# Kernel tuning notes

Measured on AMD Instinct MI355X. Metric: run time of the kernel, lower is better.

## Reference

```python
import jax, jax.numpy as jnp
import numpy as np

SEGMENT_LENGTHS = (2048, 4096, 8192)
DILATION_RATES = (1, 2, 4)


def setup_inputs() -> dict:
    key = jax.random.key(0)
    kq, kk, kv = jax.random.split(key, 3)
    b, n, h, d = 1, 8192, 12, 64
    q = jax.random.normal(kq, (b, n, h, d), dtype=jnp.float32)
    k = jax.random.normal(kk, (b, n, h, d), dtype=jnp.float32)
    v = jax.random.normal(kv, (b, n, h, d), dtype=jnp.float32)
    return {"q": q, "k": k, "v": v, "is_causal": 1}


def _dilated_attention(q, k, v, is_causal):
    # q, k, v: [b, n, h, d]
    b, n, h, d = q.shape
    num_groups = len(SEGMENT_LENGTHS)
    gh = h // num_groups  # heads per group
    scale = 1.0 / jnp.sqrt(jnp.asarray(d, dtype=q.dtype))
    qt = jnp.swapaxes(q, 1, 2)  # [b, h, n, d]
    kt = jnp.swapaxes(k, 1, 2)
    vt = jnp.swapaxes(v, 1, 2)
    group_outputs = []
    for i, (s, r) in enumerate(zip(SEGMENT_LENGTHS, DILATION_RATES)):
        hs, he = i * gh, (i + 1) * gh
        nseg = n // s
        # [b, gh, nseg, s, d]
        qs = qt[:, hs:he].reshape(b, gh, nseg, s, d)
        ks = kt[:, hs:he].reshape(b, gh, nseg, s, d)
        vs = vt[:, hs:he].reshape(b, gh, nseg, s, d)
        offset = i % r
        idx = offset + r * jnp.arange(s // r)  # dilated positions within segment
        qd = qs[:, :, :, idx]  # [b, gh, nseg, s//r, d]
        kd = ks[:, :, :, idx]
        vd = vs[:, :, :, idx]
        scores = jnp.einsum("bgnqd,bgnkd->bgnqk", qd, kd) * scale
        if is_causal:
            mask = idx[:, None] >= idx[None, :]  # same dilated indices for q/k
            scores = jnp.where(mask, scores, -jnp.inf)
        attn = jax.nn.softmax(scores, axis=-1)
        od = jnp.einsum("bgnqk,bgnkd->bgnqd", attn, vd)
        # scatter back into full segment; non-dilated positions output zero
        og = jnp.zeros((b, gh, nseg, s, d), dtype=q.dtype).at[:, :, :, idx].set(od)
        group_outputs.append(og.reshape(b, gh, n, d))
    out = jnp.concatenate(group_outputs, axis=1)  # [b, h, n, d]
    return jnp.swapaxes(out, 1, 2)  # [b, n, h, d]


def reference(q, k, v, is_causal):
    return _dilated_attention(q, k, v, bool(is_causal))
```

## Files before the change

kernel.cpp:

```cpp
#include <hip/hip_runtime.h>

typedef __attribute__((ext_vector_type(8))) __bf16 bf16x8;
typedef __attribute__((ext_vector_type(4))) __bf16 bf16x4;
typedef __attribute__((ext_vector_type(2))) __bf16 bf16x2;
typedef __attribute__((ext_vector_type(4))) float f32x4;

#define LOG2E 1.44269504088896f
#define KSWZ(t) (((t) & 7) << 4)
#define VSWZ(d) ((((d) & 7) ^ (((d) >> 3) & 7)) << 4)


__device__ __forceinline__ void inst_decode(int inst, int& head, int& sstart,
                                            int& r, int& off)
{
    if (inst < 16)      { head = inst & 3;          sstart = (inst >> 2) * 2048; r = 1; off = 0; }
    else if (inst < 24) { int j = inst - 16; head = 4 + (j & 3); sstart = (j >> 2) * 4096; r = 2; off = 1; }
    else                { head = 8 + (inst - 24);   sstart = 0;                  r = 4; off = 2; }
}

__global__ __launch_bounds__(512)
void dilattn_partial(const float* __restrict__ Qg, const float* __restrict__ Kg,
                     const float* __restrict__ Vg, float* __restrict__ Og,
                     char* __restrict__ ws, const int* __restrict__ causal_p)
{
    const int bid  = blockIdx.x;
    const int unit = (bid & 7) * 140 + (bid >> 3);
    const int inst = unit / 40;
    const int u    = 39 - (unit % 40);
    int qt, c;
    if (u < 4) { qt = u; c = 0; }
    else {
        int v = u - 4;
        if (v < 8)       { qt = 4 + (v >> 1); c = v & 1; }
        else if (v < 20) { int t = v - 8; int q3 = t / 3; qt = 8 + q3; c = t - 3 * q3; }
        else             { int t = v - 20; qt = 12 + (t >> 2); c = t & 3; }
    }
    int head, sstart, r, off;
    inst_decode(inst, head, sstart, r, off);

    const int causal = *causal_p;
    int kt_begin, kt_end;
    bool direct;
    if (causal) {
        int nkt = 2 * qt + 2;
        kt_begin = c * 8;
        kt_end   = (kt_begin + 8 < nkt) ? kt_begin + 8 : nkt;
        direct   = (qt < 4);
    } else {
        if (c) return;
        kt_begin = 0; kt_end = 32; direct = true;
    }

    const int tid  = threadIdx.x;
    const int lane = tid & 63;
    const int wave = tid >> 6;
    const int l15  = lane & 15;
    const int lhi  = lane >> 4;

    __shared__ char KV[16384];
    __shared__ __bf16 P_lds[8][16 * 64];

    const int qrow_base = qt * 128 + wave * 16;
    const float qscale = 0.125f * LOG2E;
    bf16x8 qfrag[2];
    {
        int qr = qrow_base + l15;
        long qtok = sstart + off + (long)r * qr;
        const float* qp = Qg + qtok * 768 + head * 64 + lhi * 8;
#pragma unroll
        for (int dc = 0; dc < 2; dc++) {
            f32x4 a = *(const f32x4*)(qp + dc * 32);
            f32x4 b = *(const f32x4*)(qp + dc * 32 + 4);
#pragma unroll
            for (int j = 0; j < 4; j++) {
                qfrag[dc][j]     = (__bf16)(a[j] * qscale);
                qfrag[dc][4 + j] = (__bf16)(b[j] * qscale);
            }
        }
    }

    f32x4 acc[4] = {};
    float m_run = -INFINITY;
    float l_run = 0.f;

    const bool isK = (wave < 4);
    const int t2   = tid & 255;
    const int tokK = t2 >> 2, q4 = t2 & 3;
    const int tokP = t2 >> 3, d8 = (t2 & 7) * 8;

    f32x4 r0, r1, r2, r3;

    const long gstep = (long)r * 64 * 768;
    const long vrow  = (long)r * 768;
    const float* gp0;
    {
        long tb = sstart + off + (long)r * (kt_begin * 64);
        gp0 = isK ? (Kg + (tb + (long)r * tokK) * 768 + head * 64 + q4 * 16)
                  : (Vg + (tb + (long)r * 2 * tokP) * 768 + head * 64 + d8);
    }

#define LOAD_STEP() do {                                                       \
        if (isK) {                                                             \
            r0 = *(const f32x4*)(gp0);      r1 = *(const f32x4*)(gp0 + 4);     \
            r2 = *(const f32x4*)(gp0 + 8);  r3 = *(const f32x4*)(gp0 + 12);    \
        } else {                                                               \
            const float* g1_ = gp0 + vrow;                                     \
            r0 = *(const f32x4*)(gp0);      r1 = *(const f32x4*)(gp0 + 4);     \
            r2 = *(const f32x4*)(g1_);      r3 = *(const f32x4*)(g1_ + 4);     \
        }                                                                      \
        gp0 += gstep;                                                          \
    } while (0)

#define STORE_TILE() do {                                                      \
        if (isK) {                                                             \
            char* Kb_ = KV;                                                    \
            bf16x8 w0_, w1_;                                                   \
            _Pragma("unroll")                                                  \
            for (int j = 0; j < 4; j++) {                                      \
                w0_[j] = (__bf16)r0[j]; w0_[4 + j] = (__bf16)r1[j];            \
                w1_[j] = (__bf16)r2[j]; w1_[4 + j] = (__bf16)r3[j];            \
            }                                                                  \
            int kb_ = tokK * 128 + q4 * 32;                                    \
            *(bf16x8*)(Kb_ + ((kb_)      ^ KSWZ(tokK))) = w0_;                 \
            *(bf16x8*)(Kb_ + ((kb_ + 16) ^ KSWZ(tokK))) = w1_;                 \
        } else {                                                               \
            char* Vb_ = KV + 8192;                                             \
            _Pragma("unroll")                                                  \
            for (int j = 0; j < 4; j++) {                                      \
                int d_ = d8 + j;                                               \
                bf16x2 wa_; wa_[0] = (__bf16)r0[j]; wa_[1] = (__bf16)r2[j];    \
                *(bf16x2*)(Vb_ + ((d_ * 128 + tokP * 4) ^ VSWZ(d_))) = wa_;    \
                int d2_ = d8 + 4 + j;                                          \
                bf16x2 wb_; wb_[0] = (__bf16)r1[j]; wb_[1] = (__bf16)r3[j];    \
                *(bf16x2*)(Vb_ + ((d2_ * 128 + tokP * 4) ^ VSWZ(d2_))) = wb_;  \
            }                                                                  \
        }                                                                      \
    } while (0)

    LOAD_STEP();
    STORE_TILE();
    __syncthreads();

    for (int kt = kt_begin; kt < kt_end; kt++) {
        const bool pf = (kt + 1 < kt_end);
        if (pf) LOAD_STEP();

        char* Kb = KV;
        char* Vb = KV + 8192;

        f32x4 s[4];
        __builtin_amdgcn_s_setprio(1);
#pragma unroll
        for (int nt = 0; nt < 4; nt++) {
            f32x4 cc = {};
#pragma unroll
            for (int dc = 0; dc < 2; dc++) {
                int krow = nt * 16 + l15;
                const bf16x8 kf = *(const bf16x8*)(Kb +
                    ((krow * 128 + dc * 64 + lhi * 16) ^ KSWZ(krow)));
                cc = __builtin_amdgcn_mfma_f32_16x16x32_bf16(kf, qfrag[dc], cc, 0, 0, 0);
            }
            s[nt] = cc;
        }
        __builtin_amdgcn_s_setprio(0);

        if (causal && (kt >> 1) == qt) {
            const int kofs = kt * 64 - qt * 128 - wave * 16;
#pragma unroll
            for (int nt = 0; nt < 4; nt++)
#pragma unroll
                for (int reg = 0; reg < 4; reg++)
                    if (kofs + nt * 16 + lhi * 4 + reg > l15)
                        s[nt][reg] = -INFINITY;
        }

        float a0 = fmaxf(fmaxf(s[0][0], s[0][1]), s[0][2]);
        float a1 = fmaxf(fmaxf(s[0][3], s[1][0]), s[1][1]);
        float a2 = fmaxf(fmaxf(s[1][2], s[1][3]), s[2][0]);
        float a3 = fmaxf(fmaxf(s[2][1], s[2][2]), s[2][3]);
        float a4 = fmaxf(fmaxf(s[3][0], s[3][1]), s[3][2]);
        float b0 = fmaxf(fmaxf(a0, a1), a2);
        float b1 = fmaxf(fmaxf(a3, a4), s[3][3]);
        float mt = fmaxf(b0, b1);
        mt = fmaxf(mt, __shfl_xor(mt, 16));
        mt = fmaxf(mt, __shfl_xor(mt, 32));
        if (!__all(mt - m_run <= 8.0f)) {
            float mn = fmaxf(m_run, mt);
            float sc = exp2f(m_run - mn);
            l_run *= sc;
            float scr[4];
#pragma unroll
            for (int reg = 0; reg < 4; reg++) scr[reg] = __shfl(sc, lhi * 4 + reg);
#pragma unroll
            for (int dt = 0; dt < 4; dt++)
#pragma unroll
                for (int reg = 0; reg < 4; reg++) acc[dt][reg] *= scr[reg];
            m_run = mn;
        }
        float psn[4];
#pragma unroll
        for (int nt = 0; nt < 4; nt++) {
            float p0 = exp2f(s[nt][0] - m_run);
            float p1 = exp2f(s[nt][1] - m_run);
            float p2 = exp2f(s[nt][2] - m_run);
            float p3 = exp2f(s[nt][3] - m_run);
            s[nt][0] = p0; s[nt][1] = p1; s[nt][2] = p2; s[nt][3] = p3;
            psn[nt] = (p0 + p1) + (p2 + p3);
        }
        float ps = (psn[0] + psn[1]) + (psn[2] + psn[3]);
        ps += __shfl_xor(ps, 16);
        ps += __shfl_xor(ps, 32);
        l_run += ps;

        char* pl = (char*)P_lds[wave];
        const int rs = (l15 & 7) << 4;
#pragma unroll
        for (int nt = 0; nt < 4; nt++) {
            bf16x4 pw;
#pragma unroll
            for (int reg = 0; reg < 4; reg++) pw[reg] = (__bf16)s[nt][reg];
            *(bf16x4*)(pl + ((l15 * 128 + (nt * 16 + lhi * 4) * 2) ^ rs)) = pw;
        }

        __builtin_amdgcn_s_setprio(1);
#pragma unroll
        for (int kc = 0; kc < 2; kc++) {
            const bf16x8 pfg = *(const bf16x8*)(pl +
                ((l15 * 128 + kc * 64 + lhi * 16) ^ rs));
#pragma unroll
            for (int dt = 0; dt < 4; dt++) {
                int drow = dt * 16 + l15;
                const bf16x8 vf = *(const bf16x8*)(Vb +
                    ((drow * 128 + kc * 64 + lhi * 16) ^ VSWZ(drow)));
                acc[dt] = __builtin_amdgcn_mfma_f32_16x16x32_bf16(pfg, vf, acc[dt], 0, 0, 0);
            }
        }
        __builtin_amdgcn_s_setprio(0);

        __syncthreads();
        if (pf) {
            STORE_TILE();
            __syncthreads();
        }
    }

    if (direct) {
        float lq[4];
#pragma unroll
        for (int reg = 0; reg < 4; reg++) lq[reg] = __shfl(l_run, lhi * 4 + reg);
#pragma unroll
        for (int reg = 0; reg < 4; reg++) {
            float inv = 1.0f / lq[reg];
            int qr = qrow_base + lhi * 4 + reg;
            long tok = sstart + off + (long)r * qr;
            float* op = Og + tok * 768 + head * 64 + l15;
#pragma unroll
            for (int dt = 0; dt < 4; dt++) op[dt * 16] = acc[dt][reg] * inv;
            if (r >= 2) {
                float* z1 = op - 768;
#pragma unroll
                for (int dt = 0; dt < 4; dt++) z1[dt * 16] = 0.f;
            }
            if (r == 4) {
                float* z2 = op - 2 * 768;
                float* z3 = op + 768;
#pragma unroll
                for (int dt = 0; dt < 4; dt++) { z2[dt * 16] = 0.f; z3[dt * 16] = 0.f; }
            }
        }
    } else {
        const int b  = (qt < 8)  ? (qt - 4) * 2
                     : (qt < 12) ? 8 + (qt - 8) * 3
                     :             20 + (qt - 12) * 4;
        char* slotp = ws + (size_t)(inst * 36 + b + c) * 17408;
        __bf16* so = (__bf16*)slotp;
#pragma unroll
        for (int reg = 0; reg < 4; reg++) {
            int row = wave * 16 + lhi * 4 + reg;
#pragma unroll
            for (int dt = 0; dt < 4; dt++)
                so[row * 64 + dt * 16 + l15] = (__bf16)acc[dt][reg];
        }
        if (lhi == 0) {
            float* ml = (float*)(slotp + 16384);
            ml[wave * 16 + l15]       = m_run;
            ml[128 + wave * 16 + l15] = l_run;
        }
    }
#undef LOAD_STEP
#undef STORE_TILE
}

__global__ __launch_bounds__(256)
void dilattn_merge(const char* __restrict__ ws, float* __restrict__ Og,
                   const int* __restrict__ causal_p)
{
    if (!*causal_p) return;
    const int bid  = blockIdx.x;
    const int inst = bid / 48;
    const int rem  = bid % 48;
    const int qt   = 4 + (rem >> 2);
    const int quarter = rem & 3;
    int head, sstart, r, off;
    inst_decode(inst, head, sstart, r, off);

    const int nc = (2 * qt + 9) >> 3;
    const int b  = (qt < 8)  ? (qt - 4) * 2
                 : (qt < 12) ? 8 + (qt - 8) * 3
                 :             20 + (qt - 12) * 4;
    const char* base = ws + (size_t)(inst * 36 + b) * 17408;

    const int tid = threadIdx.x;
    const int row = quarter * 32 + (tid >> 3);
    const int c8  = (tid & 7) * 8;

    float mv[4], lv[4];
    float m = -INFINITY;
#pragma unroll
    for (int c = 0; c < 4; c++) {
        if (c < nc) {
            const float* ml = (const float*)(base + c * 17408 + 16384);
            mv[c] = ml[row];
            lv[c] = ml[128 + row];
            m = fmaxf(m, mv[c]);
        }
    }
    float w[4];
    float L = 0.f;
#pragma unroll
    for (int c = 0; c < 4; c++) {
        if (c < nc) {
            w[c] = exp2f(mv[c] - m);
            L += w[c] * lv[c];
        }
    }
    const float invL = 1.0f / L;

    float o[8] = {};
#pragma unroll
    for (int c = 0; c < 4; c++) {
        if (c < nc) {
            const __bf16* ob = (const __bf16*)(base + c * 17408) + row * 64 + c8;
            bf16x8 t = *(const bf16x8*)ob;
#pragma unroll
            for (int e = 0; e < 8; e++) o[e] += w[c] * (float)t[e];
        }
    }

    long tok = sstart + off + (long)r * (qt * 128 + row);
    float* og = Og + tok * 768 + head * 64 + c8;
    f32x4 t0, t1;
#pragma unroll
    for (int e = 0; e < 4; e++) { t0[e] = o[e] * invL; t1[e] = o[4 + e] * invL; }
    *(f32x4*)(og)     = t0;
    *(f32x4*)(og + 4) = t1;

    const f32x4 zz = {};
    if (r >= 2) {
        float* z1 = og - 768;
        *(f32x4*)(z1) = zz; *(f32x4*)(z1 + 4) = zz;
    }
    if (r == 4) {
        float* z2 = og - 2 * 768;
        float* z3 = og + 768;
        *(f32x4*)(z2) = zz; *(f32x4*)(z2 + 4) = zz;
        *(f32x4*)(z3) = zz; *(f32x4*)(z3 + 4) = zz;
    }
}

extern "C" void kernel_launch(void* const* d_in, const int* in_sizes, int n_in,
                              void* d_out, int out_size, void* d_ws, size_t ws_size,
                              hipStream_t stream)
{
    const float* q = (const float*)d_in[0];
    const float* k = (const float*)d_in[1];
    const float* v = (const float*)d_in[2];
    const int* causal = (const int*)d_in[3];
    float* out = (float*)d_out;
    char* ws   = (char*)d_ws;

    dilattn_partial<<<dim3(28 * 40), dim3(512), 0, stream>>>(q, k, v, out, ws, causal);
    dilattn_merge<<<dim3(28 * 48), dim3(256), 0, stream>>>(ws, out, causal);
}
```

Measured before the change: 60.38 us.

## Process query tiles 4-7 directly without KV split, defer row-sum reduction

Query tiles 4-7 (up to 16 key tiles) now run as a single direct block instead of being split in two and merged, which cuts the partial grid from 40 to 36 units per instance and the merge grid from 48 to 32 blocks. Workspace slot indexing is remapped to match. The cross-lane shuffle reduction of the softmax row sum moves out of the inner loop and runs once after it. In exchange the longest direct blocks carry more serial work, which could leave the tail less balanced.

```diff
diff --git a/kernel.cpp b/kernel.cpp
--- a/kernel.cpp
+++ b/kernel.cpp
@@ -24,30 +24,31 @@
                      char* __restrict__ ws, const int* __restrict__ causal_p)
 {
     const int bid  = blockIdx.x;
-    const int unit = (bid & 7) * 140 + (bid >> 3);
-    const int inst = unit / 40;
-    const int u    = 39 - (unit % 40);
-    int qt, c;
-    if (u < 4) { qt = u; c = 0; }
-    else {
-        int v = u - 4;
-        if (v < 8)       { qt = 4 + (v >> 1); c = v & 1; }
-        else if (v < 20) { int t = v - 8; int q3 = t / 3; qt = 8 + q3; c = t - 3 * q3; }
-        else             { int t = v - 20; qt = 12 + (t >> 2); c = t & 3; }
-    }
+    const int unit = (bid & 7) * 126 + (bid >> 3);
+    const int inst = unit / 36;
+    const int u    = 35 - (unit % 36);
     int head, sstart, r, off;
     inst_decode(inst, head, sstart, r, off);
 
     const int causal = *causal_p;
-    int kt_begin, kt_end;
+    int qt, c, kt_begin, kt_end;
     bool direct;
     if (causal) {
+        if (u >= 32)      { qt = 39 - u; c = 0; }
+        else if (u >= 16) { qt = 12 + ((u - 16) >> 2); c = (u - 16) & 3; }
+        else if (u >= 4)  { int t = u - 4; int q3 = t / 3; qt = 8 + q3; c = t - 3 * q3; }
+        else              { qt = u; c = 0; }
+        if (u >= 32) qt = u - 28;
         int nkt = 2 * qt + 2;
-        kt_begin = c * 8;
-        kt_end   = (kt_begin + 8 < nkt) ? kt_begin + 8 : nkt;
-        direct   = (qt < 4);
+        direct = (qt < 8);
+        if (direct) { kt_begin = 0; kt_end = nkt; }
+        else {
+            kt_begin = c * 8;
+            kt_end   = (kt_begin + 8 < nkt) ? kt_begin + 8 : nkt;
+        }
     } else {
-        if (c) return;
+        if (u >= 16) return;
+        qt = u; c = 0;
         kt_begin = 0; kt_end = 32; direct = true;
     }
 
@@ -207,10 +208,7 @@
             s[nt][0] = p0; s[nt][1] = p1; s[nt][2] = p2; s[nt][3] = p3;
             psn[nt] = (p0 + p1) + (p2 + p3);
         }
-        float ps = (psn[0] + psn[1]) + (psn[2] + psn[3]);
-        ps += __shfl_xor(ps, 16);
-        ps += __shfl_xor(ps, 32);
-        l_run += ps;
+        l_run += (psn[0] + psn[1]) + (psn[2] + psn[3]);
 
         char* pl = (char*)P_lds[wave];
         const int rs = (l15 & 7) << 4;
@@ -244,6 +242,9 @@
         }
     }
 
+    l_run += __shfl_xor(l_run, 16);
+    l_run += __shfl_xor(l_run, 32);
+
     if (direct) {
         float lq[4];
 #pragma unroll
@@ -269,10 +270,8 @@
             }
         }
     } else {
-        const int b  = (qt < 8)  ? (qt - 4) * 2
-                     : (qt < 12) ? 8 + (qt - 8) * 3
-                     :             20 + (qt - 12) * 4;
-        char* slotp = ws + (size_t)(inst * 36 + b + c) * 17408;
+        const int b = (qt < 12) ? (qt - 8) * 3 : 12 + (qt - 12) * 4;
+        char* slotp = ws + (size_t)(inst * 28 + b + c) * 17408;
         __bf16* so = (__bf16*)slotp;
 #pragma unroll
         for (int reg = 0; reg < 4; reg++) {
@@ -297,18 +296,16 @@
 {
     if (!*causal_p) return;
     const int bid  = blockIdx.x;
-    const int inst = bid / 48;
-    const int rem  = bid % 48;
-    const int qt   = 4 + (rem >> 2);
+    const int inst = bid / 32;
+    const int rem  = bid % 32;
+    const int qt   = 8 + (rem >> 2);
     const int quarter = rem & 3;
     int head, sstart, r, off;
     inst_decode(inst, head, sstart, r, off);
 
-    const int nc = (2 * qt + 9) >> 3;
-    const int b  = (qt < 8)  ? (qt - 4) * 2
-                 : (qt < 12) ? 8 + (qt - 8) * 3
-                 :             20 + (qt - 12) * 4;
-    const char* base = ws + (size_t)(inst * 36 + b) * 17408;
+    const int nc = (qt < 12) ? 3 : 4;
+    const int b  = (qt < 12) ? (qt - 8) * 3 : 12 + (qt - 12) * 4;
+    const char* base = ws + (size_t)(inst * 28 + b) * 17408;
 
     const int tid = threadIdx.x;
     const int row = quarter * 32 + (tid >> 3);
@@ -379,6 +376,6 @@
     float* out = (float*)d_out;
     char* ws   = (char*)d_ws;
 
-    dilattn_partial<<<dim3(28 * 40), dim3(512), 0, stream>>>(q, k, v, out, ws, causal);
-    dilattn_merge<<<dim3(28 * 48), dim3(256), 0, stream>>>(ws, out, causal);
+    dilattn_partial<<<dim3(28 * 36), dim3(512), 0, stream>>>(q, k, v, out, ws, causal);
+    dilattn_merge<<<dim3(28 * 32), dim3(256), 0, stream>>>(ws, out, causal);
 }
```

Result: slower. 65.80 us (+9.0%).
